# Kernel tuning notes

Hardware: AMD Instinct MI355X
Metric: run time of the kernel (lower is better)

The kernel has to match this reference:

```python
import jax, jax.numpy as jnp
import numpy as np

PAD_IDX = 0

def _gru_layer(xs, W_ih, W_hh, b_ih, b_hh):
    # xs: [B, S, D]; W_ih: [3H, D]; W_hh: [3H, H]
    B = xs.shape[0]
    H = W_hh.shape[1]
    # precompute input-side gate projections for all timesteps: [S, B, 3H]
    xg = jnp.einsum('bsd,gd->sbg', xs, W_ih) + b_ih

    def step(h, xg_t):
        hg = h @ W_hh.T + b_hh                      # [B, 3H]
        xr, xz, xn = jnp.split(xg_t, 3, axis=-1)
        hr, hz, hn = jnp.split(hg, 3, axis=-1)
        r = jax.nn.sigmoid(xr + hr)
        z = jax.nn.sigmoid(xz + hz)
        n = jnp.tanh(xn + r * hn)
        h_new = (1.0 - z) * n + z * h
        return h_new, h_new

    h0 = jnp.zeros((B, H), dtype=xs.dtype)
    _, ys = jax.lax.scan(step, h0, xg)              # ys: [S, B, H]
    return jnp.transpose(ys, (1, 0, 2))             # [B, S, H]

def setup_inputs() -> dict:
    key = jax.random.key(0)
    ks = jax.random.split(key, 12)
    V, E, H = 32000, 256, 512
    B, S = 64, 512
    s_e = 1.0 / np.sqrt(H)
    inp = {
        'x': jax.random.randint(ks[0], (B, S), 0, V, dtype=jnp.int32),
        'emb': jax.random.normal(ks[1], (V, E), dtype=jnp.float32),
        'W_ih0': jax.random.uniform(ks[2], (3 * H, E), jnp.float32, -s_e, s_e),
        'W_hh0': jax.random.uniform(ks[3], (3 * H, H), jnp.float32, -s_e, s_e),
        'b_ih0': jax.random.uniform(ks[4], (3 * H,), jnp.float32, -s_e, s_e),
        'b_hh0': jax.random.uniform(ks[5], (3 * H,), jnp.float32, -s_e, s_e),
        'W_ih1': jax.random.uniform(ks[6], (3 * H, H), jnp.float32, -s_e, s_e),
        'W_hh1': jax.random.uniform(ks[7], (3 * H, H), jnp.float32, -s_e, s_e),
        'b_ih1': jax.random.uniform(ks[8], (3 * H,), jnp.float32, -s_e, s_e),
        'b_hh1': jax.random.uniform(ks[9], (3 * H,), jnp.float32, -s_e, s_e),
        'W_fc': jax.random.uniform(ks[10], (1, H), jnp.float32, -s_e, s_e),
        'b_fc': jax.random.uniform(ks[11], (1,), jnp.float32, -s_e, s_e),
    }
    return inp

def reference(x, emb, W_ih0, W_hh0, b_ih0, b_hh0, W_ih1, W_hh1, b_ih1, b_hh1, W_fc, b_fc):
    # embedding with padding_idx: pad row is zero
    emb_z = emb.at[PAD_IDX].set(0.0)
    h = emb_z[x]                                    # [B, S, E]
    h = _gru_layer(h, W_ih0, W_hh0, b_ih0, b_hh0)   # [B, S, H]
    h = _gru_layer(h, W_ih1, W_hh1, b_ih1, b_hh1)   # [B, S, H]
    final = h[:, -1, :]                             # [B, H]
    return jax.nn.sigmoid(final @ W_fc.T + b_fc)    # [B, 1]
```

## Files before the change

kernel.cpp:

```cpp
#include <hip/hip_runtime.h>
#include <math.h>

typedef short  s8v __attribute__((ext_vector_type(8)));
typedef float  f4v __attribute__((ext_vector_type(4)));
typedef unsigned long long ull;

#define S_LEN 512
#define BATCH 64
#define HID   512
#define TPB   256

#define WI0H_OFF 0L
#define WI0L_OFF 786432L
#define WH0H_OFF 1572864L
#define WH0L_OFF 3145728L
#define WI1H_OFF 4718592L
#define WI1L_OFF 6291456L
#define WH1H_OFF 7864320L
#define WH1L_OFF 9437184L
#define XEB_OFF  11010048L
#define H0R_OFF  27787264L
#define H1R_OFF  94896128L
#define NEED_FAST 95420416L

#define BAR_BYTES   4096
#define HBUF_BYTES  (HID*BATCH*4)
#define A_OFF       BAR_BYTES
#define B_OFF       (A_OFF + 2*HBUF_BYTES)
#define XE_OFF      (B_OFF + 2*HBUF_BYTES)
#define XE_BYTES    ((size_t)S_LEN*64*BATCH*16)

__device__ __forceinline__ float fexp2(float x){ return __builtin_amdgcn_exp2f(x); }
__device__ __forceinline__ float frcp (float x){ return __builtin_amdgcn_rcpf(x); }
__device__ __forceinline__ float sigm (float x){ return frcp(1.f + fexp2(-1.44269504089f*x)); }
__device__ __forceinline__ float tanhx(float x){ return 1.f - 2.f*frcp(1.f + fexp2(2.88539008178f*x)); }
__device__ __forceinline__ float sigmoid_f(float v){ return 1.0f/(1.0f + expf(-v)); }

__device__ __forceinline__ unsigned short f2bf(float f){
  unsigned int u = __float_as_uint(f);
  u = u + 0x7FFFu + ((u >> 16) & 1u);
  return (unsigned short)(u >> 16);
}
__device__ __forceinline__ float bf2f(unsigned short s){
  return __uint_as_float(((unsigned int)s) << 16);
}

__global__ void wcvt_kernel(const float* __restrict__ Wih0, const float* __restrict__ Whh0,
                            const float* __restrict__ Wih1, const float* __restrict__ Whh1,
                            char* __restrict__ ws)
{
  int idx = blockIdx.x * TPB + threadIdx.x;
  const float* src; long hi_off, lo_off; int pos;
  if (idx < 393216)       { src = Wih0; pos = idx;           hi_off = WI0H_OFF; lo_off = WI0L_OFF; }
  else if (idx < 1179648) { src = Whh0; pos = idx - 393216;  hi_off = WH0H_OFF; lo_off = WH0L_OFF; }
  else if (idx < 1966080) { src = Wih1; pos = idx - 1179648; hi_off = WI1H_OFF; lo_off = WI1L_OFF; }
  else                    { src = Whh1; pos = idx - 1966080; hi_off = WH1H_OFF; lo_off = WH1L_OFF; }
  float w = src[pos];
  unsigned short h = f2bf(w);
  unsigned short l = f2bf(w - bf2f(h));
  ((unsigned short*)(ws + hi_off))[pos] = h;
  ((unsigned short*)(ws + lo_off))[pos] = l;
}

__global__ void gather_xe_bf_kernel(const int* __restrict__ x,
                                    const float* __restrict__ emb,
                                    char* __restrict__ ws)
{
  int idx = blockIdx.x * TPB + threadIdx.x;
  int k4 = idx & 63;
  int n  = idx >> 6;
  int t = n >> 6, b = n & 63;
  int tok = x[b * S_LEN + t];
  float4 v = make_float4(0.f,0.f,0.f,0.f);
  if (tok != 0) v = ((const float4*)emb)[(size_t)tok * 64 + k4];
  unsigned int lo = (unsigned int)f2bf(v.x) | ((unsigned int)f2bf(v.y) << 16);
  unsigned int hi = (unsigned int)f2bf(v.z) | ((unsigned int)f2bf(v.w) << 16);
  ((uint2*)(ws + XEB_OFF))[(long)n * 64 + k4] = make_uint2(lo, hi);
}

__device__ __forceinline__ void st_rec(ull* p, ull v){
  __hip_atomic_store(p, v, __ATOMIC_RELAXED, __HIP_MEMORY_SCOPE_AGENT);
}

template<int NKS>
__device__ __forceinline__ void load_ct(const ull* __restrict__ sl, int b,
                                        int quad, int k0s, unsigned want,
                                        s8v* __restrict__ bf)
{
  ull d[NKS][4];
  for (;;){
    #pragma unroll
    for (int ks = 0; ks < NKS; ++ks){
      const int e = k0s + ks*4 + quad;
      const ull* p = sl + (long)(4*e)*64 + b;
      #pragma unroll
      for (int i = 0; i < 4; ++i)
        d[ks][i] = __hip_atomic_load(p + (long)i*64, __ATOMIC_RELAXED, __HIP_MEMORY_SCOPE_AGENT);
    }
    bool ok = true;
    #pragma unroll
    for (int ks = 0; ks < NKS; ++ks)
      #pragma unroll
      for (int i = 0; i < 4; ++i)
        ok = ok && ((unsigned)(d[ks][i] >> 32) == want);
    if (__all(ok)) break;
    __builtin_amdgcn_s_sleep(1);
  }
  #pragma unroll
  for (int ks = 0; ks < NKS; ++ks){
    s8v v;
    #pragma unroll
    for (int i = 0; i < 4; ++i){
      unsigned lo = (unsigned)d[ks][i];
      v[2*i]   = (short)(lo & 0xFFFFu);
      v[2*i+1] = (short)(lo >> 16);
    }
    bf[ks] = v;
  }
}

template<int NKS, int ROLE>
__device__ __forceinline__ void scan_body(
    int isL1, int rowWG, int bh, int wave, int lane, int tid, int j0, int b0,
    const s8v* __restrict__ Whi, const s8v* __restrict__ Wlo, int AKs, int k0s,
    const s8v* __restrict__ xsrc,
    const ull* __restrict__ rsrc, int slotMask,
    const float* __restrict__ bih, const float* __restrict__ bhh,
    ull* __restrict__ rout, int outMask,
    f4v* __restrict__ part)
{
  const int quad = lane >> 4, col = lane & 15;

  s8v ahi[3][NKS], alo[3][NKS];
  #pragma unroll
  for (int rt = 0; rt < 3; ++rt){
    const int row = rt*512 + j0 + col;
    #pragma unroll
    for (int ks = 0; ks < NKS; ++ks){
      const int e = row*AKs + k0s + ks*4 + quad;
      ahi[rt][ks] = Whi[e];
      alo[rt][ks] = Wlo[e];
    }
  }

  float cr[4], cz[4], cnx[4], cnh[4], hp[4];
  #pragma unroll
  for (int r4 = 0; r4 < 4; ++r4){
    int j = j0 + wave*4 + r4;
    cr[r4]  = bih[j]      + bhh[j];
    cz[r4]  = bih[512+j]  + bhh[512+j];
    cnx[r4] = bih[1024+j];
    cnh[r4] = bhh[1024+j];
    hp[r4]  = 0.f;
  }

  for (int t = 0; t < S_LEN; ++t){
    f4v acc[3][2];
    #pragma unroll
    for (int rt = 0; rt < 3; ++rt){ acc[rt][0] = (f4v)0.f; acc[rt][1] = (f4v)0.f; }

    const bool active = (ROLE != 1) || (t > 0);
    if (active){
      const ull* sl = (ROLE == 1) ? rsrc + (long)((t-1) & slotMask)*16384
                                  : rsrc + (long)(t & slotMask)*16384;
      const unsigned want = (ROLE == 1) ? (unsigned)t : (unsigned)(t+1);
      #pragma unroll
      for (int ct = 0; ct < 2; ++ct){
        s8v bf[NKS];
        if (ROLE == 0){
          const int nG = b0 + ct*16 + col;
          const long base = ((long)t*64 + nG)*32 + k0s + quad;
          #pragma unroll
          for (int ks = 0; ks < NKS; ++ks) bf[ks] = xsrc[base + ks*4];
        } else {
          load_ct<NKS>(sl, b0 + ct*16 + col, quad, k0s, want, bf);
        }
        #pragma unroll
        for (int ks = 0; ks < NKS; ++ks)
          #pragma unroll
          for (int rt = 0; rt < 3; ++rt){
            acc[rt][ct] = __builtin_amdgcn_mfma_f32_16x16x32_bf16(ahi[rt][ks], bf[ks], acc[rt][ct], 0, 0, 0);
            acc[rt][ct] = __builtin_amdgcn_mfma_f32_16x16x32_bf16(alo[rt][ks], bf[ks], acc[rt][ct], 0, 0, 0);
          }
      }
    }

    #pragma unroll
    for (int rt = 0; rt < 3; ++rt)
      #pragma unroll
      for (int ct = 0; ct < 2; ++ct)
        part[(wave*6 + rt*2 + ct)*64 + lane] = acc[rt][ct];
    __syncthreads();

    if (lane < 32){
      const int b = lane;
      const int pl = wave*16 + (b & 15);
      const int ct = b >> 4;
      f4v sr = (f4v)0.f, sz = (f4v)0.f, snx = (f4v)0.f, snh = (f4v)0.f;
      #pragma unroll
      for (int w = 0; w < 4; ++w){
        const bool inpW = isL1 ? (w < 2) : (w >= 2);
        f4v g0 = part[(w*6 + 0*2 + ct)*64 + pl];
        f4v g1 = part[(w*6 + 1*2 + ct)*64 + pl];
        f4v g2 = part[(w*6 + 2*2 + ct)*64 + pl];
        sr += g0; sz += g1;
        if (inpW) snx += g2; else snh += g2;
      }
      unsigned short hb[4];
      #pragma unroll
      for (int r4 = 0; r4 < 4; ++r4){
        float r = sigm(sr[r4] + cr[r4]);
        float z = sigm(sz[r4] + cz[r4]);
        float n = tanhx(snx[r4] + cnx[r4] + r*(snh[r4] + cnh[r4]));
        float h = n + z*(hp[r4] - n);
        hp[r4] = h;
        hb[r4] = f2bf(h);
      }
      const int slotw = t & outMask;
      const ull tg = ((ull)(unsigned)(t + 1)) << 32;
      ull* ob = rout + (long)slotw*16384 + (long)(rowWG*8 + wave*2)*64 + (b0 + b);
      st_rec(ob,      ((ull)((unsigned)hb[0] | ((unsigned)hb[1] << 16))) | tg);
      st_rec(ob + 64, ((ull)((unsigned)hb[2] | ((unsigned)hb[3] << 16))) | tg);
    }
    __syncthreads();
  }
}

__global__ __launch_bounds__(TPB, 1) void gru_mfma_kernel(
    const float* __restrict__ bih0, const float* __restrict__ bhh0,
    const float* __restrict__ bih1, const float* __restrict__ bhh1,
    const float* __restrict__ Wfc,  const float* __restrict__ bfc,
    float* __restrict__ out, char* __restrict__ ws)
{
  __shared__ f4v part[4*6*64];

  const int tid  = threadIdx.x;
  const int wg   = blockIdx.x;
  const int lane = tid & 63;
  const int wave = tid >> 6;
  const int isL1 = (wg >= 64);
  const int lw   = wg & 63;
  const int rowWG = lw >> 1;
  const int bh    = lw & 1;
  const int j0 = rowWG * 16;
  const int b0 = bh * 32;

  const s8v* wi0h = (const s8v*)(ws + WI0H_OFF); const s8v* wi0l = (const s8v*)(ws + WI0L_OFF);
  const s8v* wh0h = (const s8v*)(ws + WH0H_OFF); const s8v* wh0l = (const s8v*)(ws + WH0L_OFF);
  const s8v* wi1h = (const s8v*)(ws + WI1H_OFF); const s8v* wi1l = (const s8v*)(ws + WI1L_OFF);
  const s8v* wh1h = (const s8v*)(ws + WH1H_OFF); const s8v* wh1l = (const s8v*)(ws + WH1L_OFF);
  const s8v* xeb = (const s8v*)(ws + XEB_OFF);
  const ull* h0r = (const ull*)(ws + H0R_OFF);
  const ull* h1r = (const ull*)(ws + H1R_OFF);
  ull* h0w = (ull*)(ws + H0R_OFF);
  ull* h1w = (ull*)(ws + H1R_OFF);

  if (!isL1){
    if (wave < 2)
      scan_body<8,1>(isL1, rowWG, bh, wave, lane, tid, j0, b0,
                     wh0h, wh0l, 64, wave*32, xeb, h0r, 0x3FFFFFFF,
                     bih0, bhh0, h0w, 0x3FFFFFFF, part);
    else
      scan_body<4,0>(isL1, rowWG, bh, wave, lane, tid, j0, b0,
                     wi0h, wi0l, 32, (wave-2)*16, xeb, h0r, 0x3FFFFFFF,
                     bih0, bhh0, h0w, 0x3FFFFFFF, part);
  } else {
    if (wave < 2)
      scan_body<8,2>(isL1, rowWG, bh, wave, lane, tid, j0, b0,
                     wi1h, wi1l, 64, wave*32, xeb, h0r, 0x3FFFFFFF,
                     bih1, bhh1, h1w, 3, part);
    else
      scan_body<8,1>(isL1, rowWG, bh, wave, lane, tid, j0, b0,
                     wh1h, wh1l, 64, (wave-2)*32, xeb, h1r, 3,
                     bih1, bhh1, h1w, 3, part);
  }

  if (wg == 64 && wave == 0){
    const ull* sl = h1r + 3L*16384;
    float acc = bfc[0];
    for (int c0 = 0; c0 < 256; c0 += 32){
      ull d[32];
      for (;;){
        #pragma unroll
        for (int i = 0; i < 32; ++i)
          d[i] = __hip_atomic_load(sl + (long)(c0+i)*64 + lane,
                                   __ATOMIC_RELAXED, __HIP_MEMORY_SCOPE_AGENT);
        bool ok = true;
        #pragma unroll
        for (int i = 0; i < 32; ++i) ok = ok && ((unsigned)(d[i] >> 32) == 512u);
        if (__all(ok)) break;
        __builtin_amdgcn_s_sleep(1);
      }
      #pragma unroll
      for (int i = 0; i < 32; ++i){
        unsigned lo = (unsigned)d[i];
        int u = (c0 + i) * 2;
        acc += bf2f((unsigned short)(lo & 0xFFFFu)) * Wfc[u]
             + bf2f((unsigned short)(lo >> 16))     * Wfc[u+1];
      }
    }
    out[lane] = sigm(acc);
  }
}

__global__ void gather_xe_kernel(const int* __restrict__ x,
                                 const float* __restrict__ emb,
                                 float4* __restrict__ xe4)
{
  int idx = blockIdx.x * TPB + threadIdx.x;
  int b  = idx & 63;
  int k4 = (idx >> 6) & 63;
  int t  = idx >> 12;
  int tok = x[b * S_LEN + t];
  float4 v = make_float4(0.f, 0.f, 0.f, 0.f);
  if (tok != 0) v = ((const float4*)emb)[(size_t)tok * 64 + k4];
  xe4[idx] = v;
}

__device__ __forceinline__ void accum_vec(const float4* __restrict__ xin,
                                          const float4* __restrict__ w0,
                                          const float4* __restrict__ w1,
                                          const float4* __restrict__ w2,
                                          int n4, int lane,
                                          float& ar, float& az, float& an)
{
  #pragma unroll 4
  for (int k = 0; k < n4; ++k){
    float4 xv = xin[k * 64 + lane];
    float4 wr = w0[k], wz = w1[k], wn = w2[k];
    ar = fmaf(xv.x, wr.x, ar); az = fmaf(xv.x, wz.x, az); an = fmaf(xv.x, wn.x, an);
    ar = fmaf(xv.y, wr.y, ar); az = fmaf(xv.y, wz.y, az); an = fmaf(xv.y, wn.y, an);
    ar = fmaf(xv.z, wr.z, ar); az = fmaf(xv.z, wz.z, az); an = fmaf(xv.z, wn.z, an);
    ar = fmaf(xv.w, wr.w, ar); az = fmaf(xv.w, wz.w, az); an = fmaf(xv.w, wn.w, an);
  }
}

__device__ __forceinline__ void accum_emb(const int* __restrict__ x,
                                          const float* __restrict__ emb, int t,
                                          const float4* __restrict__ w0,
                                          const float4* __restrict__ w1,
                                          const float4* __restrict__ w2,
                                          int lane, float& ar, float& az, float& an)
{
  int tok = x[lane * S_LEN + t];
  const float4* erow = (const float4*)emb + (size_t)tok * 64;
  float m = (tok != 0) ? 1.0f : 0.0f;
  #pragma unroll 4
  for (int k = 0; k < 64; ++k){
    float4 xv = erow[k];
    float xx = xv.x*m, xy = xv.y*m, xz = xv.z*m, xw = xv.w*m;
    float4 wr = w0[k], wz = w1[k], wn = w2[k];
    ar = fmaf(xx, wr.x, ar); az = fmaf(xx, wz.x, az); an = fmaf(xx, wn.x, an);
    ar = fmaf(xy, wr.y, ar); az = fmaf(xy, wz.y, az); an = fmaf(xy, wn.y, an);
    ar = fmaf(xz, wr.z, ar); az = fmaf(xz, wz.z, az); an = fmaf(xz, wn.z, an);
    ar = fmaf(xw, wr.w, ar); az = fmaf(xw, wz.w, az); an = fmaf(xw, wn.w, an);
  }
}

__device__ __forceinline__ void stage_weights(float4* wlds, int tid, int j0, int kin4,
                                              const float* Wih, const float* Whh)
{
  const int per = 3 * (kin4 + 128);
  for (int idx = tid; idx < 4 * per; idx += TPB){
    int w = idx / per, rem = idx - w * per;
    int g = rem / (kin4 + 128), k = rem - g * (kin4 + 128);
    int row = g * HID + j0 + w;
    float4 v;
    if (k < kin4) v = ((const float4*)Wih)[(size_t)row * kin4 + k];
    else          v = ((const float4*)Whh)[(size_t)row * 128 + (k - kin4)];
    wlds[(w * 3 + g) * 256 + k] = v;
  }
}

__device__ __forceinline__ void barrier_tick(int* bar, int wg, int tid, int phase)
{
  __syncthreads();
  if (tid == 0){
    __builtin_amdgcn_fence(__ATOMIC_RELEASE, "agent");
    int* leaf = bar + 32 + (wg >> 4) * 32;
    int old = __hip_atomic_fetch_add(leaf, 1, __ATOMIC_ACQ_REL, __HIP_MEMORY_SCOPE_AGENT);
    if (old == phase * 16 + 15){
      __hip_atomic_fetch_add(bar, 1, __ATOMIC_ACQ_REL, __HIP_MEMORY_SCOPE_AGENT);
    }
    const int target = (phase + 1) * 16;
    while (__hip_atomic_load(bar, __ATOMIC_ACQUIRE, __HIP_MEMORY_SCOPE_AGENT) < target){
      __builtin_amdgcn_s_sleep(2);
    }
    __builtin_amdgcn_fence(__ATOMIC_ACQUIRE, "agent");
  }
  __syncthreads();
}

__device__ __forceinline__ void finish_store(const float4* __restrict__ hprev,
                                             float ar, float az, float anx, float anh,
                                             int lane, int j, float4* __restrict__ hout)
{
  float r  = sigmoid_f(ar);
  float zz = sigmoid_f(az);
  float n  = tanhf(fmaf(r, anh, anx));
  int fi = ((j >> 2) * 64 + lane) * 4 + (j & 3);
  float hhp = ((const float*)hprev)[fi];
  ((float*)hout)[fi] = fmaf(zz, hhp - n, n);
}

__global__ __launch_bounds__(TPB) void gru_persist_kernel(
    const int*   __restrict__ x,    const float* __restrict__ emb,
    const float* __restrict__ Wih0, const float* __restrict__ Whh0,
    const float* __restrict__ bih0, const float* __restrict__ bhh0,
    const float* __restrict__ Wih1, const float* __restrict__ Whh1,
    const float* __restrict__ bih1, const float* __restrict__ bhh1,
    const float* __restrict__ Wfc,  const float* __restrict__ bfc,
    float* __restrict__ out, int* __restrict__ bar,
    float4* __restrict__ A0, float4* __restrict__ A1,
    float4* __restrict__ B0, float4* __restrict__ B1,
    const float4* __restrict__ xe4, int use_xe)
{
  __shared__ float4 wlds[3072];
  const int tid  = threadIdx.x;
  const int wg   = blockIdx.x;
  const int lane = tid & 63;
  const int wave = tid >> 6;
  const bool isL1 = (wg >= 128);
  const int j0   = (isL1 ? wg - 128 : wg) * 4;
  const int kin4 = isL1 ? 128 : 64;

  stage_weights(wlds, tid, j0, kin4, isL1 ? Wih1 : Wih0, isL1 ? Whh1 : Whh0);
  __syncthreads();

  const int j = j0 + wave;
  const float* bih = isL1 ? bih1 : bih0;
  const float* bhh = isL1 ? bhh1 : bhh0;
  const float br  = bih[j]        + bhh[j];
  const float bz  = bih[j + 512]  + bhh[j + 512];
  const float bnx = bih[j + 1024];
  const float bnh = bhh[j + 1024];

  const float4* w0 = &wlds[(wave * 3 + 0) * 256];
  const float4* w1 = &wlds[(wave * 3 + 1) * 256];
  const float4* w2 = &wlds[(wave * 3 + 2) * 256];

  float4* A[2] = {A0, A1};
  float4* B[2] = {B0, B1};

  for (int t = 0; t <= S_LEN; ++t){
    if (!isL1){
      if (t < S_LEN){
        const float4* hprev = A[(t + 1) & 1];
        float ar = br, az = bz, anx = bnx, anh = bnh;
        if (use_xe) accum_vec(xe4 + (size_t)t * 4096, w0, w1, w2, 64, lane, ar, az, anx);
        else        accum_emb(x, emb, t, w0, w1, w2, lane, ar, az, anx);
        accum_vec(hprev, w0 + 64, w1 + 64, w2 + 64, 128, lane, ar, az, anh);
        finish_store(hprev, ar, az, anx, anh, lane, j, A[t & 1]);
      }
    } else if (t >= 1){
      const int u = t - 1;
      const float4* xin   = A[u & 1];
      const float4* hprev = B[(u + 1) & 1];
      float ar = br, az = bz, anx = bnx, anh = bnh;
      accum_vec(xin,   w0,       w1,       w2,       128, lane, ar, az, anx);
      accum_vec(hprev, w0 + 128, w1 + 128, w2 + 128, 128, lane, ar, az, anh);
      finish_store(hprev, ar, az, anx, anh, lane, j, B[u & 1]);
    }
    barrier_tick(bar, wg, tid, t);
  }

  if (wg == 0 && wave == 0){
    float acc = bfc[0];
    const float4* h1 = B[1];
    const float4* wf = (const float4*)Wfc;
    #pragma unroll 4
    for (int k = 0; k < 128; ++k){
      float4 hv = h1[k * 64 + lane];
      float4 wv = wf[k];
      acc = fmaf(hv.x, wv.x, acc); acc = fmaf(hv.y, wv.y, acc);
      acc = fmaf(hv.z, wv.z, acc); acc = fmaf(hv.w, wv.w, acc);
    }
    out[lane] = sigmoid_f(acc);
  }
}

extern "C" void kernel_launch(void* const* d_in, const int* in_sizes, int n_in,
                              void* d_out, int out_size, void* d_ws, size_t ws_size,
                              hipStream_t stream)
{
  (void)in_sizes; (void)n_in; (void)out_size;
  const int*   x    = (const int*)  d_in[0];
  const float* emb  = (const float*)d_in[1];
  const float* Wih0 = (const float*)d_in[2];
  const float* Whh0 = (const float*)d_in[3];
  const float* bih0 = (const float*)d_in[4];
  const float* bhh0 = (const float*)d_in[5];
  const float* Wih1 = (const float*)d_in[6];
  const float* Whh1 = (const float*)d_in[7];
  const float* bih1 = (const float*)d_in[8];
  const float* bhh1 = (const float*)d_in[9];
  const float* Wfc  = (const float*)d_in[10];
  const float* bfc  = (const float*)d_in[11];
  float* out = (float*)d_out;
  char* ws = (char*)d_ws;

  if (ws_size >= (size_t)NEED_FAST){
    wcvt_kernel<<<2752512 / TPB, TPB, 0, stream>>>(Wih0, Whh0, Wih1, Whh1, ws);
    gather_xe_bf_kernel<<<2097152 / TPB, TPB, 0, stream>>>(x, emb, ws);
    gru_mfma_kernel<<<128, TPB, 0, stream>>>(bih0, bhh0, bih1, bhh1, Wfc, bfc, out, ws);
  } else {
    int*    bar = (int*)ws;
    float4* A0  = (float4*)(ws + A_OFF);
    float4* A1  = (float4*)(ws + A_OFF + HBUF_BYTES);
    float4* B0  = (float4*)(ws + B_OFF);
    float4* B1  = (float4*)(ws + B_OFF + HBUF_BYTES);
    float4* xe4 = (float4*)(ws + XE_OFF);
    const int use_xe = (ws_size >= (size_t)XE_OFF + XE_BYTES) ? 1 : 0;
    hipMemsetAsync(ws, 0, XE_OFF, stream);
    if (use_xe){
      gather_xe_kernel<<<(S_LEN * 64 * BATCH) / TPB, TPB, 0, stream>>>(x, emb, xe4);
    }
    gru_persist_kernel<<<256, TPB, 0, stream>>>(
        x, emb, Wih0, Whh0, bih0, bhh0, Wih1, Whh1, bih1, bhh1, Wfc, bfc,
        out, bar, A0, A1, B0, B1, xe4, use_xe);
  }
}
```

Measured before the change: 2.040 ms.

## Double-buffer partial sums, drop second barrier, pre-poll recurrence flags

Double-buffers the LDS partial-sum array by timestep parity, which makes the trailing __syncthreads per step unnecessary, and replaces the remaining one with an explicit lgkmcnt wait plus s_barrier. Before loading operands, consumer waves poll a set of recurrence flags with relaxed atomic loads and s_sleep until the wanted timestep tag appears. The gate math is also split into two halves so the first packed store goes out before the second pair is computed. This aims to cut per-step barrier and spin cost in the persistent recurrent loop, at the price of doubled LDS use and an extra polling pass that could add latency.

```diff
diff --git a/kernel.cpp b/kernel.cpp
--- a/kernel.cpp
+++ b/kernel.cpp
@@ -164,6 +164,20 @@
       const ull* sl = (ROLE == 1) ? rsrc + (long)((t-1) & slotMask)*16384
                                   : rsrc + (long)(t & slotMask)*16384;
       const unsigned want = (ROLE == 1) ? (unsigned)t : (unsigned)(t+1);
+
+      if (ROLE != 0){
+        const ull* pp = sl + (long)(4*k0s + 4*(lane & 31) + 3)*64 + (b0 + (lane & 31));
+        for (;;){
+          bool pok = true;
+          if (lane < 32){
+            ull pv = __hip_atomic_load(pp, __ATOMIC_RELAXED, __HIP_MEMORY_SCOPE_AGENT);
+            pok = ((unsigned)(pv >> 32) == want);
+          }
+          if (__all(pok)) break;
+          __builtin_amdgcn_s_sleep(1);
+        }
+      }
+
       #pragma unroll
       for (int ct = 0; ct < 2; ++ct){
         s8v bf[NKS];
@@ -185,12 +199,16 @@
       }
     }
 
+    f4v* pb = part + (t & 1)*(4*6*64);
     #pragma unroll
     for (int rt = 0; rt < 3; ++rt)
       #pragma unroll
       for (int ct = 0; ct < 2; ++ct)
-        part[(wave*6 + rt*2 + ct)*64 + lane] = acc[rt][ct];
-    __syncthreads();
+        pb[(wave*6 + rt*2 + ct)*64 + lane] = acc[rt][ct];
+
+    asm volatile("s_waitcnt lgkmcnt(0)" ::: "memory");
+    __builtin_amdgcn_s_barrier();
+    asm volatile("" ::: "memory");
 
     if (lane < 32){
       const int b = lane;
@@ -200,29 +218,31 @@
       #pragma unroll
       for (int w = 0; w < 4; ++w){
         const bool inpW = isL1 ? (w < 2) : (w >= 2);
-        f4v g0 = part[(w*6 + 0*2 + ct)*64 + pl];
-        f4v g1 = part[(w*6 + 1*2 + ct)*64 + pl];
-        f4v g2 = part[(w*6 + 2*2 + ct)*64 + pl];
+        f4v g0 = pb[(w*6 + 0*2 + ct)*64 + pl];
+        f4v g1 = pb[(w*6 + 1*2 + ct)*64 + pl];
+        f4v g2 = pb[(w*6 + 2*2 + ct)*64 + pl];
         sr += g0; sz += g1;
         if (inpW) snx += g2; else snh += g2;
-      }
-      unsigned short hb[4];
-      #pragma unroll
-      for (int r4 = 0; r4 < 4; ++r4){
-        float r = sigm(sr[r4] + cr[r4]);
-        float z = sigm(sz[r4] + cz[r4]);
-        float n = tanhx(snx[r4] + cnx[r4] + r*(snh[r4] + cnh[r4]));
-        float h = n + z*(hp[r4] - n);
-        hp[r4] = h;
-        hb[r4] = f2bf(h);
       }
       const int slotw = t & outMask;
       const ull tg = ((ull)(unsigned)(t + 1)) << 32;
       ull* ob = rout + (long)slotw*16384 + (long)(rowWG*8 + wave*2)*64 + (b0 + b);
-      st_rec(ob,      ((ull)((unsigned)hb[0] | ((unsigned)hb[1] << 16))) | tg);
-      st_rec(ob + 64, ((ull)((unsigned)hb[2] | ((unsigned)hb[3] << 16))) | tg);
-    }
-    __syncthreads();
+      #pragma unroll
+      for (int pr = 0; pr < 2; ++pr){
+        unsigned short h2[2];
+        #pragma unroll
+        for (int q = 0; q < 2; ++q){
+          const int r4 = pr*2 + q;
+          float r = sigm(sr[r4] + cr[r4]);
+          float z = sigm(sz[r4] + cz[r4]);
+          float n = tanhx(snx[r4] + cnx[r4] + r*(snh[r4] + cnh[r4]));
+          float h = n + z*(hp[r4] - n);
+          hp[r4] = h;
+          h2[q] = f2bf(h);
+        }
+        st_rec(ob + pr*64, ((ull)((unsigned)h2[0] | ((unsigned)h2[1] << 16))) | tg);
+      }
+    }
   }
 }
 
@@ -232,7 +252,7 @@
     const float* __restrict__ Wfc,  const float* __restrict__ bfc,
     float* __restrict__ out, char* __restrict__ ws)
 {
-  __shared__ f4v part[4*6*64];
+  __shared__ f4v part[2*4*6*64];
 
   const int tid  = threadIdx.x;
   const int wg   = blockIdx.x;
```

Measured after the change: 2.289 ms. 1.12x slower.
